# Optimization experiments

Hardware: AMD Instinct MI355X
Metric: run time of the kernel (lower is better)

The kernel has to match this reference:

```python
import jax, jax.numpy as jnp
import numpy as np

B, S, E, H = 2, 2048, 1024, 16
DH = E // H  # 64


def setup_inputs() -> dict:
    key = jax.random.key(0)
    ks = jax.random.split(key, 5)
    scale = 1.0 / np.sqrt(E)
    x = jax.random.normal(ks[0], (B, S, E), dtype=jnp.float32)
    # stacked per-head kqv Linear weights: out = x @ Wkqv[h] + bkqv[h], producing (k, q, v) chunks
    Wkqv = jax.random.normal(ks[1], (H, E, 3 * DH), dtype=jnp.float32) * scale
    bkqv = jax.random.normal(ks[2], (H, 3 * DH), dtype=jnp.float32) * scale
    Wo = jax.random.normal(ks[3], (E, E), dtype=jnp.float32) * scale
    bo = jax.random.normal(ks[4], (E,), dtype=jnp.float32) * scale
    return {"x": x, "Wkqv": Wkqv, "bkqv": bkqv, "Wo": Wo, "bo": bo}


def reference(x, Wkqv, bkqv, Wo, bo):
    b, s, e = x.shape
    h, _, f = Wkqv.shape
    dh = f // 3
    # per-head projection, fused over heads: [b, h, s, 3*dh]
    kqv = jnp.einsum('bse,hef->bhsf', x, Wkqv) + bkqv[None, :, None, :]
    # chunk order in the original is k, q, v
    k, q, v = jnp.split(kqv, 3, axis=-1)
    scores = jnp.einsum('bhqd,bhkd->bhqk', q, k) / jnp.sqrt(jnp.asarray(dh, x.dtype))
    causal = jnp.tril(jnp.ones((s, s), dtype=bool))  # slice of the tril buffer
    scores = jnp.where(causal[None, None], scores, -jnp.inf)
    weights = jax.nn.softmax(scores, axis=-1)
    sa = jnp.einsum('bhqk,bhkd->bhqd', weights, v)
    # concat heads along feature dim (head order preserved)
    sa = sa.transpose(0, 2, 1, 3).reshape(b, s, h * dh)
    return sa @ Wo + bo
```

## Files before the change

kernel.cpp:

```cpp
#include <hip/hip_runtime.h>
#include <hip/hip_bf16.h>

typedef __attribute__((ext_vector_type(8))) short bf16x8;
typedef __attribute__((ext_vector_type(4))) float f32x4;
typedef __attribute__((ext_vector_type(2))) unsigned u32x2;
typedef __attribute__((ext_vector_type(4))) unsigned u32x4;
typedef unsigned short u16;

#define NEG_INF (-__builtin_inff())

__device__ __forceinline__ void gload16(const void* g, void* l) {
  __builtin_amdgcn_global_load_lds(
      (const __attribute__((address_space(1))) void*)g,
      (__attribute__((address_space(3))) void*)l, 16, 0, 0);
}

__device__ __forceinline__ u16 f2b(float f) {
  union { float f; unsigned u; } v;
  v.f = f;
  unsigned r = v.u + 0x7fff + ((v.u >> 16) & 1);
  return (u16)(r >> 16);
}

__device__ __forceinline__ unsigned cvt_pk_bf16(float a, float b) {
  unsigned r;
  asm("v_cvt_pk_bf16_f32 %0, %1, %2" : "=v"(r) : "v"(a), "v"(b));
  return r;
}

__global__ __launch_bounds__(256) void prep_kernel(
    const float* __restrict__ x, u16* __restrict__ xb,
    const float* __restrict__ Wkqv, u16* __restrict__ WkqvT,
    const float* __restrict__ Wo, u16* __restrict__ WoT) {
  __shared__ u16 t[32][33];
  const int bid = blockIdx.x;
  const int tid = threadIdx.x;
  if (bid < 4096) {
    const int i = bid * 256 + tid;
    float4 v = ((const float4*)x)[i];
    ushort2 a = {f2b(v.x), f2b(v.y)}, b = {f2b(v.z), f2b(v.w)};
    ((ushort2*)xb)[i * 2] = a;
    ((ushort2*)xb)[i * 2 + 1] = b;
    return;
  }
  const int tx = tid & 31, ty = tid >> 5;
  const float* src;
  u16* dst;
  int R, C, bx_, by;
  if (bid < 7168) {
    const int tt = bid - 4096;
    const int bz = tt / 192, rem = tt % 192;
    by = rem / 6; bx_ = rem % 6; R = 1024; C = 192;
    src = Wkqv + (size_t)bz * R * C;
    dst = WkqvT + (size_t)bz * R * C;
  } else {
    const int tt = bid - 7168;
    by = tt >> 5; bx_ = tt & 31; R = 1024; C = 1024;
    src = Wo; dst = WoT;
  }
  const int c0 = bx_ * 32, r0 = by * 32;
  for (int i = ty; i < 32; i += 8)
    t[i][tx] = f2b(src[(size_t)(r0 + i) * C + c0 + tx]);
  __syncthreads();
  for (int i = ty; i < 32; i += 8)
    dst[(size_t)(c0 + i) * R + r0 + tx] = t[tx][i];
}

__device__ __forceinline__ void gemm_mainloop_128(
    const __hip_bfloat16* __restrict__ A, const __hip_bfloat16* __restrict__ Bt,
    int K, int m0, int n0, f32x4 acc[4][4], char* AsB, char* BsB) {
  const int tid = threadIdx.x;
  const int wave = tid >> 6, lane = tid & 63;
  const int lhi = lane >> 4, llo = lane & 15;
  const int wr = wave >> 1, wc = wave & 1;
  f32x4 z = {0.f, 0.f, 0.f, 0.f};
#pragma unroll
  for (int i = 0; i < 4; i++)
#pragma unroll
    for (int j = 0; j < 4; j++) acc[i][j] = z;

#define GSTAGE(c, kk)                                                          \
  {                                                                            \
    char* AsW = AsB + (c)*8192;                                                \
    char* BsW = BsB + (c)*8192;                                                \
    _Pragma("unroll") for (int i = 0; i < 2; i++) {                            \
      int cb = i * 256 + wave * 64;                                            \
      int cq = cb + lane;                                                      \
      gload16(A + ((size_t)(m0 + (cq >> 2)) * K + (kk) + (cq & 3) * 8),        \
              AsW + cb * 16);                                                  \
      gload16(Bt + ((size_t)(n0 + (cq >> 2)) * K + (kk) + (cq & 3) * 8),       \
              BsW + cb * 16);                                                  \
    }                                                                          \
  }

  GSTAGE(0, 0);
  int cur = 0;
  const int nk = K >> 5;
  for (int t = 0; t < nk; t++) {
    if (t + 1 < nk) {
      GSTAGE(cur ^ 1, (t + 1) * 32);
      asm volatile("s_waitcnt vmcnt(4)" ::: "memory");
    } else {
      asm volatile("s_waitcnt vmcnt(0)" ::: "memory");
    }
    __builtin_amdgcn_s_barrier();
    __builtin_amdgcn_sched_barrier(0);

    const char* Ar = AsB + cur * 8192;
    const char* Br = BsB + cur * 8192;
    bf16x8 a[4], b[4];
#pragma unroll
    for (int m4 = 0; m4 < 4; m4++)
      a[m4] = *(const bf16x8*)(Ar + (wr * 64 + m4 * 16 + llo) * 64 + lhi * 16);
#pragma unroll
    for (int n4 = 0; n4 < 4; n4++)
      b[n4] = *(const bf16x8*)(Br + (wc * 64 + n4 * 16 + llo) * 64 + lhi * 16);
#pragma unroll
    for (int m4 = 0; m4 < 4; m4++)
#pragma unroll
      for (int n4 = 0; n4 < 4; n4++)
        acc[m4][n4] =
            __builtin_amdgcn_mfma_f32_16x16x32_bf16(a[m4], b[n4], acc[m4][n4], 0, 0, 0);
    __builtin_amdgcn_sched_barrier(0);
    __builtin_amdgcn_s_barrier();
    cur ^= 1;
  }
#undef GSTAGE
}

__device__ __forceinline__ void gemm_mainloop_64x128(
    const __hip_bfloat16* __restrict__ A, const __hip_bfloat16* __restrict__ Bt,
    int K, int m0, int n0, f32x4 acc[2][4], char* AsB, char* BsB) {
  const int tid = threadIdx.x;
  const int wave = tid >> 6, lane = tid & 63;
  const int lhi = lane >> 4, llo = lane & 15;
  const int wr = wave >> 1, wc = wave & 1;
  f32x4 z = {0.f, 0.f, 0.f, 0.f};
#pragma unroll
  for (int i = 0; i < 2; i++)
#pragma unroll
    for (int j = 0; j < 4; j++) acc[i][j] = z;

#define GSTAGE64(c, kk)                                                        \
  {                                                                            \
    char* AsW = AsB + (c)*4096;                                                \
    char* BsW = BsB + (c)*8192;                                                \
    gload16(A + ((size_t)(m0 + (tid >> 2)) * K + (kk) + (tid & 3) * 8),        \
            AsW + (wave * 64) * 16);                                           \
    _Pragma("unroll") for (int i = 0; i < 2; i++) {                            \
      int cb = i * 256 + wave * 64;                                            \
      int cq = cb + lane;                                                      \
      gload16(Bt + ((size_t)(n0 + (cq >> 2)) * K + (kk) + (cq & 3) * 8),       \
              BsW + cb * 16);                                                  \
    }                                                                          \
  }

  GSTAGE64(0, 0);
  int cur = 0;
  const int nk = K >> 5;
  for (int t = 0; t < nk; t++) {
    if (t + 1 < nk) {
      GSTAGE64(cur ^ 1, (t + 1) * 32);
      asm volatile("s_waitcnt vmcnt(3)" ::: "memory");
    } else {
      asm volatile("s_waitcnt vmcnt(0)" ::: "memory");
    }
    __builtin_amdgcn_s_barrier();
    __builtin_amdgcn_sched_barrier(0);

    const char* Ar = AsB + cur * 4096;
    const char* Br = BsB + cur * 8192;
    bf16x8 a[2], b[4];
#pragma unroll
    for (int m2 = 0; m2 < 2; m2++)
      a[m2] = *(const bf16x8*)(Ar + (wr * 32 + m2 * 16 + llo) * 64 + lhi * 16);
#pragma unroll
    for (int n4 = 0; n4 < 4; n4++)
      b[n4] = *(const bf16x8*)(Br + (wc * 64 + n4 * 16 + llo) * 64 + lhi * 16);
#pragma unroll
    for (int m2 = 0; m2 < 2; m2++)
#pragma unroll
      for (int n4 = 0; n4 < 4; n4++)
        acc[m2][n4] =
            __builtin_amdgcn_mfma_f32_16x16x32_bf16(a[m2], b[n4], acc[m2][n4], 0, 0, 0);
    __builtin_amdgcn_sched_barrier(0);
    __builtin_amdgcn_s_barrier();
    cur ^= 1;
  }
#undef GSTAGE64
}

__global__ __launch_bounds__(256) void kqv_gemm(
    const __hip_bfloat16* __restrict__ x, const __hip_bfloat16* __restrict__ WT,
    const float* __restrict__ bkqv, __hip_bfloat16* __restrict__ Qb,
    __hip_bfloat16* __restrict__ Kb, __hip_bfloat16* __restrict__ Vt) {
  __shared__ __align__(16) char As[16384];
  __shared__ __align__(16) char Bs[16384];
  const int m0 = blockIdx.y * 128, n0 = blockIdx.x * 128;
  f32x4 acc[4][4];
  gemm_mainloop_128(x, WT, 1024, m0, n0, acc, As, Bs);

  const int tid = threadIdx.x, wave = tid >> 6, lane = tid & 63;
  const int lhi = lane >> 4, llo = lane & 15;
  const int wr = wave >> 1, wc = wave & 1;
#pragma unroll
  for (int m4 = 0; m4 < 4; m4++)
#pragma unroll
    for (int n4 = 0; n4 < 4; n4++)
#pragma unroll
      for (int r = 0; r < 4; r++) {
        int mg = m0 + wr * 64 + m4 * 16 + lhi * 4 + r;
        int ng = n0 + wc * 64 + n4 * 16 + llo;
        int b = mg >> 11, s = mg & 2047;
        int h = ng / 192, f = ng % 192;
        float v = acc[m4][n4][r] + bkqv[h * 192 + f];
        int chunk = f >> 6, d = f & 63;
        size_t bh = (size_t)(b * 16 + h);
        if (chunk == 0)
          Kb[(bh * 2048 + s) * 64 + d] = __float2bfloat16(v);
        else if (chunk == 1)
          Qb[(bh * 2048 + s) * 64 + d] = __float2bfloat16(v * 0.180336880f);
        else
          Vt[(bh * 64 + d) * 2048 + s] = __float2bfloat16(v);
      }
}

__global__ __launch_bounds__(512) void attn_kernel(
    const __hip_bfloat16* __restrict__ Qb, const __hip_bfloat16* __restrict__ Kb,
    const __hip_bfloat16* __restrict__ Vt, __hip_bfloat16* __restrict__ SA) {
  __shared__ __align__(16) char lds[32768];
  const int orig = blockIdx.x;
  const int xcd = orig & 7, j = orig >> 3;
  const int bh = xcd * 4 + (j & 3);
  const int t = 15 - (j >> 2);
  const int qoff = t * 128;
  const int nt = 2 * t + 2;
  const int b = bh >> 4, h = bh & 15;
  const int tid = threadIdx.x, wave = tid >> 6, lane = tid & 63;
  const int lhi = lane >> 4, llo = lane & 15;
  const int lhi4 = lhi * 4;

  const __hip_bfloat16* qp =
      Qb + ((size_t)bh * 2048 + qoff + wave * 16 + llo) * 64 + lhi * 8;
  bf16x8 q0 = *(const bf16x8*)qp, q1 = *(const bf16x8*)(qp + 32);

  const char* Kg = (const char*)(Kb + (size_t)bh * 2048 * 64);
  const char* Vg = (const char*)(Vt + (size_t)bh * 64 * 2048);

  f32x4 z = {0.f, 0.f, 0.f, 0.f};
  f32x4 o[4];
  float m_s = NEG_INF, l_s = 0.f;
#pragma unroll
  for (int i = 0; i < 4; i++) o[i] = z;
  const int qg = qoff + wave * 16 + llo;
  const int qg0 = qoff + wave * 16 + lhi4;
  const int wave_rmax = qoff + wave * 16 + 15;

#define STAGE(c, k0)                                                          \
  {                                                                           \
    char* KsW = lds + (c)*8192;                                               \
    char* VsW = lds + 16384 + (c)*8192;                                       \
    const int ch = tid;                                                       \
    int soff = (ch * 16) ^ (((ch >> 3) & 7) << 4);                            \
    gload16(Kg + (size_t)(k0)*128 + soff, KsW + wave * 1024);                 \
    int dd = ch >> 3, c8 = ch & 7;                                            \
    int boff = (c8 * 16) ^ ((dd & 7) << 4);                                   \
    gload16(Vg + (size_t)dd * 4096 + (size_t)(k0)*2 + boff, VsW + wave * 1024);\
  }

  STAGE(0, 0);
  int cur = 0;

  for (int T = 0; T < nt; T++) {
    if (T + 1 < nt) {
      STAGE(cur ^ 1, (T + 1) * 64);
      asm volatile("s_waitcnt vmcnt(2)" ::: "memory");
    } else {
      asm volatile("s_waitcnt vmcnt(0)" ::: "memory");
    }
    __builtin_amdgcn_s_barrier();
    __builtin_amdgcn_sched_barrier(0);

    const int k0 = T * 64;
    if (k0 <= wave_rmax) {
      const bool masked = (k0 + 63 > wave_rmax - 15);
      const char* KsB = lds + cur * 8192;
      const char* VsB = lds + 16384 + cur * 8192;

      f32x4 s[4] = {z, z, z, z};
#pragma unroll
      for (int jj = 0; jj < 4; jj++) {
        const int row = jj * 16 + llo;
        const int rx = (row & 7) << 4;
        bf16x8 bk0 = *(const bf16x8*)(KsB + ((row * 128 + lhi * 16) ^ rx));
        bf16x8 bk1 = *(const bf16x8*)(KsB + ((row * 128 + 64 + lhi * 16) ^ rx));
        s[jj] = __builtin_amdgcn_mfma_f32_16x16x32_bf16(bk0, q0, s[jj], 0, 0, 0);
        s[jj] = __builtin_amdgcn_mfma_f32_16x16x32_bf16(bk1, q1, s[jj], 0, 0, 0);
      }

      if (masked) {
#pragma unroll
        for (int jj = 0; jj < 4; jj++)
#pragma unroll
          for (int r = 0; r < 4; r++)
            if (k0 + jj * 16 + lhi4 + r > qg) s[jj][r] = NEG_INF;
      }
      float pmax = s[0][0];
#pragma unroll
      for (int jj = 0; jj < 4; jj++)
#pragma unroll
        for (int r = 0; r < 4; r++) pmax = fmaxf(pmax, s[jj][r]);
      {
        union { float f; unsigned u; } pu;
        pu.f = pmax;
        u32x2 sp = __builtin_amdgcn_permlane32_swap(pu.u, pu.u, false, false);
        float m1 = fmaxf(__uint_as_float(sp.x), __uint_as_float(sp.y));
        union { float f; unsigned u; } mu;
        mu.f = m1;
        u32x2 tp = __builtin_amdgcn_permlane16_swap(mu.u, mu.u, false, false);
        pmax = fmaxf(__uint_as_float(tp.x), __uint_as_float(tp.y));
      }
      if (!__all(pmax - m_s <= 5.0f)) {
        const float mn = fmaxf(m_s, pmax);
        const float sc = __builtin_exp2f(m_s - mn);
        m_s = mn;
        l_s *= sc;
#pragma unroll
        for (int r = 0; r < 4; r++) {
          const float scr = __shfl(sc, lhi4 + r);
#pragma unroll
          for (int n4 = 0; n4 < 4; n4++) o[n4][r] *= scr;
        }
      }

      unsigned pk[4][2];
      float ps = 0.f;
#pragma unroll
      for (int jj = 0; jj < 4; jj++) {
        float p0 = __builtin_exp2f(s[jj][0] - m_s);
        float p1 = __builtin_exp2f(s[jj][1] - m_s);
        float p2 = __builtin_exp2f(s[jj][2] - m_s);
        float p3 = __builtin_exp2f(s[jj][3] - m_s);
        ps += (p0 + p1) + (p2 + p3);
        pk[jj][0] = cvt_pk_bf16(p0, p1);
        pk[jj][1] = cvt_pk_bf16(p2, p3);
      }
      l_s += ps;

      u32x4 a0w, a1w;
#pragma unroll
      for (int u = 0; u < 2; u++) {
        u32x2 sp = __builtin_amdgcn_permlane32_swap(pk[0][u], pk[1][u], false, false);
        u32x2 tp = __builtin_amdgcn_permlane16_swap(sp.x, sp.y, false, false);
        a0w[u] = tp.x;
        a0w[u + 2] = tp.y;
      }
#pragma unroll
      for (int u = 0; u < 2; u++) {
        u32x2 sp = __builtin_amdgcn_permlane32_swap(pk[2][u], pk[3][u], false, false);
        u32x2 tp = __builtin_amdgcn_permlane16_swap(sp.x, sp.y, false, false);
        a1w[u] = tp.x;
        a1w[u + 2] = tp.y;
      }
      bf16x8 ap0 = __builtin_bit_cast(bf16x8, a0w);
      bf16x8 ap1 = __builtin_bit_cast(bf16x8, a1w);

#pragma unroll
      for (int n4 = 0; n4 < 4; n4++) {
        const int d = n4 * 16 + llo;
        const int dx = (d & 7) << 4;
        bf16x8 bv0 = *(const bf16x8*)(VsB + ((d * 128 + lhi * 16) ^ dx));
        bf16x8 bv1 = *(const bf16x8*)(VsB + ((d * 128 + 64 + lhi * 16) ^ dx));
        o[n4] = __builtin_amdgcn_mfma_f32_16x16x32_bf16(ap0, bv0, o[n4], 0, 0, 0);
        o[n4] = __builtin_amdgcn_mfma_f32_16x16x32_bf16(ap1, bv1, o[n4], 0, 0, 0);
      }
    }
    __builtin_amdgcn_sched_barrier(0);
    __builtin_amdgcn_s_barrier();
    cur ^= 1;
  }

  {
    union { float f; unsigned u; } lu;
    lu.f = l_s;
    u32x2 sp = __builtin_amdgcn_permlane32_swap(lu.u, lu.u, false, false);
    float l1 = __uint_as_float(sp.x) + __uint_as_float(sp.y);
    union { float f; unsigned u; } l2u;
    l2u.f = l1;
    u32x2 tp = __builtin_amdgcn_permlane16_swap(l2u.u, l2u.u, false, false);
    const float l = __uint_as_float(tp.x) + __uint_as_float(tp.y);
    const float inv = 1.f / l;
#pragma unroll
    for (int r = 0; r < 4; r++) {
      const float invr = __shfl(inv, lhi4 + r);
      const size_t ob = ((size_t)b * 2048 + qg0 + r) * 1024 + h * 64;
#pragma unroll
      for (int n4 = 0; n4 < 4; n4++)
        SA[ob + n4 * 16 + llo] = __float2bfloat16(o[n4][r] * invr);
    }
  }
#undef STAGE
}

__global__ __launch_bounds__(256) void out_gemm(
    const __hip_bfloat16* __restrict__ SA, const __hip_bfloat16* __restrict__ WoT,
    const float* __restrict__ bo, float* __restrict__ out) {
  __shared__ __align__(16) char As[8192];
  __shared__ __align__(16) char Bs[16384];
  const int m0 = blockIdx.y * 64, n0 = blockIdx.x * 128;
  f32x4 acc[2][4];
  gemm_mainloop_64x128(SA, WoT, 1024, m0, n0, acc, As, Bs);

  const int tid = threadIdx.x, wave = tid >> 6, lane = tid & 63;
  const int lhi = lane >> 4, llo = lane & 15;
  const int wr = wave >> 1, wc = wave & 1;
#pragma unroll
  for (int m2 = 0; m2 < 2; m2++)
#pragma unroll
    for (int n4 = 0; n4 < 4; n4++)
#pragma unroll
      for (int r = 0; r < 4; r++) {
        int mg = m0 + wr * 32 + m2 * 16 + lhi * 4 + r;
        int ng = n0 + wc * 64 + n4 * 16 + llo;
        out[(size_t)mg * 1024 + ng] = acc[m2][n4][r] + bo[ng];
      }
}

extern "C" void kernel_launch(void* const* d_in, const int* in_sizes, int n_in,
                              void* d_out, int out_size, void* d_ws, size_t ws_size,
                              hipStream_t stream) {
  const float* x = (const float*)d_in[0];
  const float* Wkqv = (const float*)d_in[1];
  const float* bkqv = (const float*)d_in[2];
  const float* Wo = (const float*)d_in[3];
  const float* bo = (const float*)d_in[4];
  float* out = (float*)d_out;

  char* w = (char*)d_ws;
  __hip_bfloat16* WkqvT = (__hip_bfloat16*)(w);
  __hip_bfloat16* WoT = (__hip_bfloat16*)(w + 6291456);
  __hip_bfloat16* Qb = (__hip_bfloat16*)(w + 8388608);
  __hip_bfloat16* Kb = (__hip_bfloat16*)(w + 16777216);
  __hip_bfloat16* Vt = (__hip_bfloat16*)(w + 25165824);
  __hip_bfloat16* SAb = (__hip_bfloat16*)(w + 33554432);
  __hip_bfloat16* xb = (__hip_bfloat16*)(w + 41943040);

  prep_kernel<<<8192, 256, 0, stream>>>(x, (u16*)xb, Wkqv, (u16*)WkqvT,
                                        Wo, (u16*)WoT);
  kqv_gemm<<<dim3(24, 32), 256, 0, stream>>>(xb, WkqvT, bkqv, Qb, Kb, Vt);
  attn_kernel<<<512, 512, 0, stream>>>(Qb, Kb, Vt, SAb);
  out_gemm<<<dim3(8, 64), 256, 0, stream>>>(SAb, WoT, bo, out);
}
```

Before: 119.7 us.

## Shrink attention query tile to 64 rows and widen KV tile to 128

The attention kernel now uses 4-wave blocks over 64 query rows each, launching 1024 blocks instead of 512. Each pipeline stage loads a 128-key K/V tile into 64KB of double-buffered LDS, so there are half as many barrier and staging iterations per key range. Each tile is processed as two 64-key halves, skipping any half that is fully masked. The aim is finer causal load balancing and less per-iteration synchronisation. The cost is double the LDS per block, which may reduce occupancy, and more redundant K/V loading across blocks.

```diff
diff --git a/kernel.cpp b/kernel.cpp
--- a/kernel.cpp
+++ b/kernel.cpp
@@ -225,23 +225,21 @@
       }
 }
 
-__global__ __launch_bounds__(512) void attn_kernel(
+__global__ __launch_bounds__(256) void attn_kernel(
     const __hip_bfloat16* __restrict__ Qb, const __hip_bfloat16* __restrict__ Kb,
     const __hip_bfloat16* __restrict__ Vt, __hip_bfloat16* __restrict__ SA) {
-  __shared__ __align__(16) char lds[32768];
+  __shared__ __align__(16) char lds[65536];
   const int orig = blockIdx.x;
-  const int xcd = orig & 7, j = orig >> 3;
-  const int bh = xcd * 4 + (j & 3);
-  const int t = 15 - (j >> 2);
-  const int qoff = t * 128;
-  const int nt = 2 * t + 2;
+  const int bh = (orig & 7) * 4 + ((orig >> 3) & 3);
+  const int qt = 31 - (orig >> 5);
+  const int nt = (qt >> 1) + 1;
   const int b = bh >> 4, h = bh & 15;
   const int tid = threadIdx.x, wave = tid >> 6, lane = tid & 63;
   const int lhi = lane >> 4, llo = lane & 15;
   const int lhi4 = lhi * 4;
 
   const __hip_bfloat16* qp =
-      Qb + ((size_t)bh * 2048 + qoff + wave * 16 + llo) * 64 + lhi * 8;
+      Qb + ((size_t)bh * 2048 + qt * 64 + wave * 16 + llo) * 64 + lhi * 8;
   bf16x8 q0 = *(const bf16x8*)qp, q1 = *(const bf16x8*)(qp + 32);
 
   const char* Kg = (const char*)(Kb + (size_t)bh * 2048 * 64);
@@ -252,20 +250,23 @@
   float m_s = NEG_INF, l_s = 0.f;
 #pragma unroll
   for (int i = 0; i < 4; i++) o[i] = z;
-  const int qg = qoff + wave * 16 + llo;
-  const int qg0 = qoff + wave * 16 + lhi4;
-  const int wave_rmax = qoff + wave * 16 + 15;
+  const int qg = qt * 64 + wave * 16 + llo;
+  const int qg0 = qt * 64 + wave * 16 + lhi4;
+  const int wave_rmax = qt * 64 + wave * 16 + 15;
 
 #define STAGE(c, k0)                                                          \
   {                                                                           \
-    char* KsW = lds + (c)*8192;                                               \
-    char* VsW = lds + 16384 + (c)*8192;                                       \
-    const int ch = tid;                                                       \
-    int soff = (ch * 16) ^ (((ch >> 3) & 7) << 4);                            \
-    gload16(Kg + (size_t)(k0)*128 + soff, KsW + wave * 1024);                 \
-    int dd = ch >> 3, c8 = ch & 7;                                            \
-    int boff = (c8 * 16) ^ ((dd & 7) << 4);                                   \
-    gload16(Vg + (size_t)dd * 4096 + (size_t)(k0)*2 + boff, VsW + wave * 1024);\
+    char* KsW = lds + (c)*16384;                                              \
+    char* VsW = lds + 32768 + (c)*16384;                                      \
+    _Pragma("unroll") for (int i = 0; i < 4; i++) {                           \
+      int ch = i * 256 + tid;                                                 \
+      int soff = (ch * 16) ^ (((ch >> 3) & 7) << 4);                          \
+      gload16(Kg + (size_t)(k0)*128 + soff, KsW + (i * 256 + wave * 64) * 16);\
+      int dd = ch >> 4, c16 = ch & 15;                                        \
+      int boff = (c16 >> 3) * 128 + (((c16 & 7) * 16) ^ ((dd & 7) << 4));     \
+      gload16(Vg + (size_t)dd * 4096 + (size_t)(k0)*2 + boff,                 \
+              VsW + (i * 256 + wave * 64) * 16);                              \
+    }                                                                         \
   }
 
   STAGE(0, 0);
@@ -273,25 +274,28 @@
 
   for (int T = 0; T < nt; T++) {
     if (T + 1 < nt) {
-      STAGE(cur ^ 1, (T + 1) * 64);
-      asm volatile("s_waitcnt vmcnt(2)" ::: "memory");
+      STAGE(cur ^ 1, (T + 1) * 128);
+      asm volatile("s_waitcnt vmcnt(8)" ::: "memory");
     } else {
       asm volatile("s_waitcnt vmcnt(0)" ::: "memory");
     }
     __builtin_amdgcn_s_barrier();
     __builtin_amdgcn_sched_barrier(0);
 
-    const int k0 = T * 64;
-    if (k0 <= wave_rmax) {
-      const bool masked = (k0 + 63 > wave_rmax - 15);
-      const char* KsB = lds + cur * 8192;
-      const char* VsB = lds + 16384 + cur * 8192;
+    const char* KsB = lds + cur * 16384;
+    const char* VsB = lds + 32768 + cur * 16384;
+
+#pragma unroll
+    for (int hf = 0; hf < 2; hf++) {
+      const int k0h = T * 128 + hf * 64;
+      if (k0h > wave_rmax) continue;
+      const bool masked = (k0h + 63 > wave_rmax - 15);
 
       f32x4 s[4] = {z, z, z, z};
 #pragma unroll
       for (int jj = 0; jj < 4; jj++) {
-        const int row = jj * 16 + llo;
-        const int rx = (row & 7) << 4;
+        const int row = hf * 64 + jj * 16 + llo;
+        const int rx = (llo & 7) << 4;
         bf16x8 bk0 = *(const bf16x8*)(KsB + ((row * 128 + lhi * 16) ^ rx));
         bf16x8 bk1 = *(const bf16x8*)(KsB + ((row * 128 + 64 + lhi * 16) ^ rx));
         s[jj] = __builtin_amdgcn_mfma_f32_16x16x32_bf16(bk0, q0, s[jj], 0, 0, 0);
@@ -303,7 +307,7 @@
         for (int jj = 0; jj < 4; jj++)
 #pragma unroll
           for (int r = 0; r < 4; r++)
-            if (k0 + jj * 16 + lhi4 + r > qg) s[jj][r] = NEG_INF;
+            if (k0h + jj * 16 + lhi4 + r > qg) s[jj][r] = NEG_INF;
       }
       float pmax = s[0][0];
 #pragma unroll
@@ -369,8 +373,8 @@
       for (int n4 = 0; n4 < 4; n4++) {
         const int d = n4 * 16 + llo;
         const int dx = (d & 7) << 4;
-        bf16x8 bv0 = *(const bf16x8*)(VsB + ((d * 128 + lhi * 16) ^ dx));
-        bf16x8 bv1 = *(const bf16x8*)(VsB + ((d * 128 + 64 + lhi * 16) ^ dx));
+        bf16x8 bv0 = *(const bf16x8*)(VsB + ((d * 256 + hf * 128 + lhi * 16) ^ dx));
+        bf16x8 bv1 = *(const bf16x8*)(VsB + ((d * 256 + hf * 128 + 64 + lhi * 16) ^ dx));
         o[n4] = __builtin_amdgcn_mfma_f32_16x16x32_bf16(ap0, bv0, o[n4], 0, 0, 0);
         o[n4] = __builtin_amdgcn_mfma_f32_16x16x32_bf16(ap1, bv1, o[n4], 0, 0, 0);
       }
@@ -448,6 +452,6 @@
   prep_kernel<<<8192, 256, 0, stream>>>(x, (u16*)xb, Wkqv, (u16*)WkqvT,
                                         Wo, (u16*)WoT);
   kqv_gemm<<<dim3(24, 32), 256, 0, stream>>>(xb, WkqvT, bkqv, Qb, Kb, Vt);
-  attn_kernel<<<512, 512, 0, stream>>>(Qb, Kb, Vt, SAb);
+  attn_kernel<<<1024, 256, 0, stream>>>(Qb, Kb, Vt, SAb);
   out_gemm<<<dim3(8, 64), 256, 0, stream>>>(SAb, WoT, bo, out);
 }
```

Result: slower. 123.9 us (+3.5%).

## Give each attention wave two query sub-tiles to reuse K/V LDS reads

Applied to the files above, without the earlier changes.

The attention kernel now runs 4 waves per block instead of 8, and each wave handles 32 query rows as two 16-row sub-tiles. Both sub-tiles share the same K and V fragments read from LDS, which halves the LDS traffic per MFMA and exposes more independent MFMA work per wave. MFMA sections are wrapped in s_setprio, and each thread now issues two staging loads for K and two for V per tile. The trade-off is higher register pressure, fewer waves per block to hide latency, and some divergence where the first sub-tile is inactive on the diagonal.

```diff
diff --git a/kernel.cpp b/kernel.cpp
--- a/kernel.cpp
+++ b/kernel.cpp
@@ -225,47 +225,118 @@
       }
 }
 
-__global__ __launch_bounds__(512) void attn_kernel(
+__device__ __forceinline__ void softmax_pack(
+    f32x4* s, bool masked, int k0, int qg, int lhi4,
+    float& m_s, float& l_s, f32x4* o, bf16x8& ap0, bf16x8& ap1) {
+  if (masked) {
+#pragma unroll
+    for (int jj = 0; jj < 4; jj++)
+#pragma unroll
+      for (int r = 0; r < 4; r++)
+        if (k0 + jj * 16 + lhi4 + r > qg) s[jj][r] = NEG_INF;
+  }
+  float pmax = s[0][0];
+#pragma unroll
+  for (int jj = 0; jj < 4; jj++)
+#pragma unroll
+    for (int r = 0; r < 4; r++) pmax = fmaxf(pmax, s[jj][r]);
+  {
+    union { float f; unsigned u; } pu;
+    pu.f = pmax;
+    u32x2 sp = __builtin_amdgcn_permlane32_swap(pu.u, pu.u, false, false);
+    float m1 = fmaxf(__uint_as_float(sp.x), __uint_as_float(sp.y));
+    union { float f; unsigned u; } mu;
+    mu.f = m1;
+    u32x2 tp = __builtin_amdgcn_permlane16_swap(mu.u, mu.u, false, false);
+    pmax = fmaxf(__uint_as_float(tp.x), __uint_as_float(tp.y));
+  }
+  if (!__all(pmax - m_s <= 5.0f)) {
+    const float mn = fmaxf(m_s, pmax);
+    const float sc = __builtin_exp2f(m_s - mn);
+    m_s = mn;
+    l_s *= sc;
+#pragma unroll
+    for (int r = 0; r < 4; r++) {
+      const float scr = __shfl(sc, lhi4 + r);
+#pragma unroll
+      for (int n4 = 0; n4 < 4; n4++) o[n4][r] *= scr;
+    }
+  }
+  unsigned pk[4][2];
+  float ps = 0.f;
+#pragma unroll
+  for (int jj = 0; jj < 4; jj++) {
+    float p0 = __builtin_exp2f(s[jj][0] - m_s);
+    float p1 = __builtin_exp2f(s[jj][1] - m_s);
+    float p2 = __builtin_exp2f(s[jj][2] - m_s);
+    float p3 = __builtin_exp2f(s[jj][3] - m_s);
+    ps += (p0 + p1) + (p2 + p3);
+    pk[jj][0] = cvt_pk_bf16(p0, p1);
+    pk[jj][1] = cvt_pk_bf16(p2, p3);
+  }
+  l_s += ps;
+
+  u32x4 a0w, a1w;
+#pragma unroll
+  for (int u = 0; u < 2; u++) {
+    u32x2 sp = __builtin_amdgcn_permlane32_swap(pk[0][u], pk[1][u], false, false);
+    u32x2 tp = __builtin_amdgcn_permlane16_swap(sp.x, sp.y, false, false);
+    a0w[u] = tp.x;
+    a0w[u + 2] = tp.y;
+  }
+#pragma unroll
+  for (int u = 0; u < 2; u++) {
+    u32x2 sp = __builtin_amdgcn_permlane32_swap(pk[2][u], pk[3][u], false, false);
+    u32x2 tp = __builtin_amdgcn_permlane16_swap(sp.x, sp.y, false, false);
+    a1w[u] = tp.x;
+    a1w[u + 2] = tp.y;
+  }
+  ap0 = __builtin_bit_cast(bf16x8, a0w);
+  ap1 = __builtin_bit_cast(bf16x8, a1w);
+}
+
+__global__ __launch_bounds__(256) void attn_kernel(
     const __hip_bfloat16* __restrict__ Qb, const __hip_bfloat16* __restrict__ Kb,
     const __hip_bfloat16* __restrict__ Vt, __hip_bfloat16* __restrict__ SA) {
   __shared__ __align__(16) char lds[32768];
   const int orig = blockIdx.x;
-  const int xcd = orig & 7, j = orig >> 3;
-  const int bh = xcd * 4 + (j & 3);
-  const int t = 15 - (j >> 2);
-  const int qoff = t * 128;
-  const int nt = 2 * t + 2;
+  const int bh = (orig & 7) * 4 + ((orig >> 3) & 3);
+  const int qblk = 15 - (orig >> 5);
+  const int nt = 2 * qblk + 2;
   const int b = bh >> 4, h = bh & 15;
   const int tid = threadIdx.x, wave = tid >> 6, lane = tid & 63;
   const int lhi = lane >> 4, llo = lane & 15;
   const int lhi4 = lhi * 4;
+  const int wbase = qblk * 128 + wave * 32;
 
   const __hip_bfloat16* qp =
-      Qb + ((size_t)bh * 2048 + qoff + wave * 16 + llo) * 64 + lhi * 8;
-  bf16x8 q0 = *(const bf16x8*)qp, q1 = *(const bf16x8*)(qp + 32);
+      Qb + ((size_t)bh * 2048 + wbase + llo) * 64 + lhi * 8;
+  bf16x8 qA0 = *(const bf16x8*)qp, qA1 = *(const bf16x8*)(qp + 32);
+  bf16x8 qB0 = *(const bf16x8*)(qp + 16 * 64), qB1 = *(const bf16x8*)(qp + 16 * 64 + 32);
 
   const char* Kg = (const char*)(Kb + (size_t)bh * 2048 * 64);
   const char* Vg = (const char*)(Vt + (size_t)bh * 64 * 2048);
 
   f32x4 z = {0.f, 0.f, 0.f, 0.f};
-  f32x4 o[4];
-  float m_s = NEG_INF, l_s = 0.f;
-#pragma unroll
-  for (int i = 0; i < 4; i++) o[i] = z;
-  const int qg = qoff + wave * 16 + llo;
-  const int qg0 = qoff + wave * 16 + lhi4;
-  const int wave_rmax = qoff + wave * 16 + 15;
+  f32x4 o0[4], o1[4];
+  float m0 = NEG_INF, l0 = 0.f, m1 = NEG_INF, l1 = 0.f;
+#pragma unroll
+  for (int i = 0; i < 4; i++) { o0[i] = z; o1[i] = z; }
+  const int qg_0 = wbase + llo, qg_1 = wbase + 16 + llo;
 
 #define STAGE(c, k0)                                                          \
   {                                                                           \
     char* KsW = lds + (c)*8192;                                               \
     char* VsW = lds + 16384 + (c)*8192;                                       \
-    const int ch = tid;                                                       \
-    int soff = (ch * 16) ^ (((ch >> 3) & 7) << 4);                            \
-    gload16(Kg + (size_t)(k0)*128 + soff, KsW + wave * 1024);                 \
-    int dd = ch >> 3, c8 = ch & 7;                                            \
-    int boff = (c8 * 16) ^ ((dd & 7) << 4);                                   \
-    gload16(Vg + (size_t)dd * 4096 + (size_t)(k0)*2 + boff, VsW + wave * 1024);\
+    _Pragma("unroll") for (int i = 0; i < 2; i++) {                           \
+      int ch = i * 256 + tid;                                                 \
+      int soff = (ch * 16) ^ (((ch >> 3) & 7) << 4);                          \
+      gload16(Kg + (size_t)(k0)*128 + soff, KsW + (i * 256 + wave * 64) * 16);\
+      int dd = ch >> 3, c8 = ch & 7;                                          \
+      int boff = (c8 * 16) ^ ((dd & 7) << 4);                                 \
+      gload16(Vg + (size_t)dd * 4096 + (size_t)(k0)*2 + boff,                 \
+              VsW + (i * 256 + wave * 64) * 16);                              \
+    }                                                                         \
   }
 
   STAGE(0, 0);
@@ -274,7 +345,7 @@
   for (int T = 0; T < nt; T++) {
     if (T + 1 < nt) {
       STAGE(cur ^ 1, (T + 1) * 64);
-      asm volatile("s_waitcnt vmcnt(2)" ::: "memory");
+      asm volatile("s_waitcnt vmcnt(4)" ::: "memory");
     } else {
       asm volatile("s_waitcnt vmcnt(0)" ::: "memory");
     }
@@ -282,88 +353,33 @@
     __builtin_amdgcn_sched_barrier(0);
 
     const int k0 = T * 64;
-    if (k0 <= wave_rmax) {
-      const bool masked = (k0 + 63 > wave_rmax - 15);
+    if (k0 <= wbase + 31) {
+      const bool act0 = (k0 <= wbase + 15);
+      const bool msk0 = (k0 + 63 > wbase);
+      const bool msk1 = (k0 + 63 > wbase + 16);
       const char* KsB = lds + cur * 8192;
       const char* VsB = lds + 16384 + cur * 8192;
 
-      f32x4 s[4] = {z, z, z, z};
+      f32x4 s[4] = {z, z, z, z}, t[4] = {z, z, z, z};
 #pragma unroll
       for (int jj = 0; jj < 4; jj++) {
         const int row = jj * 16 + llo;
-        const int rx = (row & 7) << 4;
+        const int rx = (llo & 7) << 4;
         bf16x8 bk0 = *(const bf16x8*)(KsB + ((row * 128 + lhi * 16) ^ rx));
         bf16x8 bk1 = *(const bf16x8*)(KsB + ((row * 128 + 64 + lhi * 16) ^ rx));
-        s[jj] = __builtin_amdgcn_mfma_f32_16x16x32_bf16(bk0, q0, s[jj], 0, 0, 0);
-        s[jj] = __builtin_amdgcn_mfma_f32_16x16x32_bf16(bk1, q1, s[jj], 0, 0, 0);
+        __builtin_amdgcn_s_setprio(1);
+        if (act0) {
+          s[jj] = __builtin_amdgcn_mfma_f32_16x16x32_bf16(bk0, qA0, s[jj], 0, 0, 0);
+          s[jj] = __builtin_amdgcn_mfma_f32_16x16x32_bf16(bk1, qA1, s[jj], 0, 0, 0);
+        }
+        t[jj] = __builtin_amdgcn_mfma_f32_16x16x32_bf16(bk0, qB0, t[jj], 0, 0, 0);
+        t[jj] = __builtin_amdgcn_mfma_f32_16x16x32_bf16(bk1, qB1, t[jj], 0, 0, 0);
+        __builtin_amdgcn_s_setprio(0);
       }
 
-      if (masked) {
-#pragma unroll
-        for (int jj = 0; jj < 4; jj++)
-#pragma unroll
-          for (int r = 0; r < 4; r++)
-            if (k0 + jj * 16 + lhi4 + r > qg) s[jj][r] = NEG_INF;
-      }
-      float pmax = s[0][0];
-#pragma unroll
-      for (int jj = 0; jj < 4; jj++)
-#pragma unroll
-        for (int r = 0; r < 4; r++) pmax = fmaxf(pmax, s[jj][r]);
-      {
-        union { float f; unsigned u; } pu;
-        pu.f = pmax;
-        u32x2 sp = __builtin_amdgcn_permlane32_swap(pu.u, pu.u, false, false);
-        float m1 = fmaxf(__uint_as_float(sp.x), __uint_as_float(sp.y));
-        union { float f; unsigned u; } mu;
-        mu.f = m1;
-        u32x2 tp = __builtin_amdgcn_permlane16_swap(mu.u, mu.u, false, false);
-        pmax = fmaxf(__uint_as_float(tp.x), __uint_as_float(tp.y));
-      }
-      if (!__all(pmax - m_s <= 5.0f)) {
-        const float mn = fmaxf(m_s, pmax);
-        const float sc = __builtin_exp2f(m_s - mn);
-        m_s = mn;
-        l_s *= sc;
-#pragma unroll
-        for (int r = 0; r < 4; r++) {
-          const float scr = __shfl(sc, lhi4 + r);
-#pragma unroll
-          for (int n4 = 0; n4 < 4; n4++) o[n4][r] *= scr;
-        }
-      }
-
-      unsigned pk[4][2];
-      float ps = 0.f;
-#pragma unroll
-      for (int jj = 0; jj < 4; jj++) {
-        float p0 = __builtin_exp2f(s[jj][0] - m_s);
-        float p1 = __builtin_exp2f(s[jj][1] - m_s);
-        float p2 = __builtin_exp2f(s[jj][2] - m_s);
-        float p3 = __builtin_exp2f(s[jj][3] - m_s);
-        ps += (p0 + p1) + (p2 + p3);
-        pk[jj][0] = cvt_pk_bf16(p0, p1);
-        pk[jj][1] = cvt_pk_bf16(p2, p3);
-      }
-      l_s += ps;
-
-      u32x4 a0w, a1w;
-#pragma unroll
-      for (int u = 0; u < 2; u++) {
-        u32x2 sp = __builtin_amdgcn_permlane32_swap(pk[0][u], pk[1][u], false, false);
-        u32x2 tp = __builtin_amdgcn_permlane16_swap(sp.x, sp.y, false, false);
-        a0w[u] = tp.x;
-        a0w[u + 2] = tp.y;
-      }
-#pragma unroll
-      for (int u = 0; u < 2; u++) {
-        u32x2 sp = __builtin_amdgcn_permlane32_swap(pk[2][u], pk[3][u], false, false);
-        u32x2 tp = __builtin_amdgcn_permlane16_swap(sp.x, sp.y, false, false);
-        a1w[u] = tp.x;
-        a1w[u + 2] = tp.y;
-      }
-      bf16x8 ap0 = __builtin_bit_cast(bf16x8, a0w);
-      bf16x8 ap1 = __builtin_bit_cast(bf16x8, a1w);
+      bf16x8 ap0_0, ap1_0, ap0_1, ap1_1;
+      if (act0) softmax_pack(s, msk0, k0, qg_0, lhi4, m0, l0, o0, ap0_0, ap1_0);
+      softmax_pack(t, msk1, k0, qg_1, lhi4, m1, l1, o1, ap0_1, ap1_1);
 
 #pragma unroll
       for (int n4 = 0; n4 < 4; n4++) {
@@ -371,8 +387,14 @@
         const int dx = (d & 7) << 4;
         bf16x8 bv0 = *(const bf16x8*)(VsB + ((d * 128 + lhi * 16) ^ dx));
         bf16x8 bv1 = *(const bf16x8*)(VsB + ((d * 128 + 64 + lhi * 16) ^ dx));
-        o[n4] = __builtin_amdgcn_mfma_f32_16x16x32_bf16(ap0, bv0, o[n4], 0, 0, 0);
-        o[n4] = __builtin_amdgcn_mfma_f32_16x16x32_bf16(ap1, bv1, o[n4], 0, 0, 0);
+        __builtin_amdgcn_s_setprio(1);
+        if (act0) {
+          o0[n4] = __builtin_amdgcn_mfma_f32_16x16x32_bf16(ap0_0, bv0, o0[n4], 0, 0, 0);
+          o0[n4] = __builtin_amdgcn_mfma_f32_16x16x32_bf16(ap1_0, bv1, o0[n4], 0, 0, 0);
+        }
+        o1[n4] = __builtin_amdgcn_mfma_f32_16x16x32_bf16(ap0_1, bv0, o1[n4], 0, 0, 0);
+        o1[n4] = __builtin_amdgcn_mfma_f32_16x16x32_bf16(ap1_1, bv1, o1[n4], 0, 0, 0);
+        __builtin_amdgcn_s_setprio(0);
       }
     }
     __builtin_amdgcn_sched_barrier(0);
@@ -380,13 +402,17 @@
     cur ^= 1;
   }
 
-  {
+#pragma unroll
+  for (int c = 0; c < 2; c++) {
+    float l_s = c ? l1 : l0;
+    f32x4* o = c ? o1 : o0;
+    const int qg0 = wbase + 16 * c + lhi4;
     union { float f; unsigned u; } lu;
     lu.f = l_s;
     u32x2 sp = __builtin_amdgcn_permlane32_swap(lu.u, lu.u, false, false);
-    float l1 = __uint_as_float(sp.x) + __uint_as_float(sp.y);
+    float ls1 = __uint_as_float(sp.x) + __uint_as_float(sp.y);
     union { float f; unsigned u; } l2u;
-    l2u.f = l1;
+    l2u.f = ls1;
     u32x2 tp = __builtin_amdgcn_permlane16_swap(l2u.u, l2u.u, false, false);
     const float l = __uint_as_float(tp.x) + __uint_as_float(tp.y);
     const float inv = 1.f / l;
@@ -448,6 +474,6 @@
   prep_kernel<<<8192, 256, 0, stream>>>(x, (u16*)xb, Wkqv, (u16*)WkqvT,
                                         Wo, (u16*)WoT);
   kqv_gemm<<<dim3(24, 32), 256, 0, stream>>>(xb, WkqvT, bkqv, Qb, Kb, Vt);
-  attn_kernel<<<512, 512, 0, stream>>>(Qb, Kb, Vt, SAb);
+  attn_kernel<<<512, 256, 0, stream>>>(Qb, Kb, Vt, SAb);
   out_gemm<<<dim3(8, 64), 256, 0, stream>>>(SAb, WoT, bo, out);
 }
```

Result: slower. 137.4 us (+14.8%).
